# Kernel tuning notes

Measured on AMD Instinct MI355X. Metric: run time of the kernel, lower is better.

## Reference

```python
import jax, jax.numpy as jnp
import numpy as np

B, N, D, G = 128, 36, 512, 2  # batch, num_bboxs, wrd_embed_size, num_glimpses
NEG = -1e10


def setup_inputs() -> dict:
    key = jax.random.key(0)
    k1, k2, k3 = jax.random.split(key, 3)
    obj_repr = jax.random.normal(k1, (B, N, D), dtype=jnp.float32)
    # attn_glimpse[0]: nn.Linear(num_bboxs * wrd_embed_size, num_glimpses)
    W = jax.random.normal(k2, (G, N * D), dtype=jnp.float32) * 0.02
    b = jnp.zeros((G,), dtype=jnp.float32)
    bboxs_mask = jax.random.randint(k3, (B, N), 0, 2).astype(bool)
    bboxs_mask = bboxs_mask.at[:, 0].set(True)  # at least one valid box per row
    return {"obj_repr": obj_repr, "W": W, "b": b, "bboxs_mask": bboxs_mask}


def reference(obj_repr, W, b, bboxs_mask):
    """Faithful port of QGenModel.self_diff_attention."""
    Bv, Nv, Dv = obj_repr.shape
    # pairwise object differences, gated by the query object: [B, N, N, D]
    diff = obj_repr[:, :, None, :] * (obj_repr[:, :, None, :] - obj_repr[:, None, :, :])
    flat = diff.reshape(Bv, Nv, Nv * Dv)              # [B, N, N*D]
    logits = flat @ W.T + b                            # [B, N, G]
    logits = jnp.where(bboxs_mask[:, :, None], logits, NEG)
    weight = jax.nn.softmax(logits, axis=1)            # softmax over box axis (dim=1)
    # weight.transpose(1,2) @ obj_repr  ->  [B, G, D]
    vis_repr = jnp.einsum('bng,bnd->bgd', weight, obj_repr)
    return vis_repr.reshape(Bv, -1)                    # [B, G*D]
```

## Files before the change

kernel.cpp:

```cpp
#include <hip/hip_runtime.h>
#include <hip/hip_bf16.h>


#define QB 128
#define QN 36
#define QD 512
#define QG 2

__global__ __launch_bounds__(QD) void qgen_self_diff_attn(
    const float* __restrict__ obj,
    const float* __restrict__ W,
    const float* __restrict__ bias,
    const int* __restrict__ mask,
    float* __restrict__ out)
{
    __shared__ float s_T[QD];
    __shared__ float s_S[QD];
    __shared__ float s_logit[QN];
    __shared__ float s_w[QN];

    const int bid = blockIdx.x;
    const int b = bid & (QB - 1);
    const int g = bid >> 7;
    const int t = threadIdx.x;
    const int wave = t >> 6;
    const int lane = t & 63;

    const float* ob = obj + (size_t)b * QN * QD;
    const float* wg = W + (size_t)g * QN * QD;

    float o[QN];
    float T = 0.f, S = 0.f;
    #pragma unroll
    for (int m = 0; m < QN; ++m) {
        o[m] = ob[m * QD + t];
        float w = wg[m * QD + t];
        T = fmaf(w, o[m], T);
        S += w;
    }
    s_T[t] = T;
    s_S[t] = S;
    __syncthreads();

    for (int n = wave; n < QN; n += 8) {
        float a = 0.f;
        #pragma unroll
        for (int k = 0; k < QD / 64; ++k) {
            int d = lane + k * 64;
            float ov = ob[n * QD + d];
            a += ov * ov * s_S[d] - ov * s_T[d];
        }
        #pragma unroll
        for (int off = 32; off; off >>= 1)
            a += __shfl_down(a, off);
        if (lane == 0) {
            bool mk = mask[b * QN + n] != 0;
            s_logit[n] = mk ? a + bias[g] : -1e10f;
        }
    }
    __syncthreads();

    if (wave == 0) {
        float v = (lane < QN) ? s_logit[lane] : -1e30f;
        float mx = v;
        #pragma unroll
        for (int off = 32; off; off >>= 1)
            mx = fmaxf(mx, __shfl_xor(mx, off));
        float e = (lane < QN) ? __expf(v - mx) : 0.f;
        float sum = e;
        #pragma unroll
        for (int off = 32; off; off >>= 1)
            sum += __shfl_xor(sum, off);
        if (lane < QN) s_w[lane] = e / sum;
    }
    __syncthreads();

    float v = 0.f;
    #pragma unroll
    for (int n = 0; n < QN; ++n)
        v = fmaf(s_w[n], o[n], v);
    out[(size_t)b * QG * QD + (size_t)g * QD + t] = v;
}

extern "C" void kernel_launch(void* const* d_in, const int* in_sizes, int n_in,
                              void* d_out, int out_size, void* d_ws, size_t ws_size,
                              hipStream_t stream) {
    const float* obj  = (const float*)d_in[0];
    const float* W    = (const float*)d_in[1];
    const float* bias = (const float*)d_in[2];
    const int*   mask = (const int*)d_in[3];
    float* out = (float*)d_out;

    qgen_self_diff_attn<<<QB * QG, QD, 0, stream>>>(obj, W, bias, mask, out);
}
```

Before: 68.05 us.

## Repartition work as float4 row-groups, reuse register tiles for logits

Each block's 512 threads now split into 4 row groups of 128 threads. Each thread holds 9 objects as float4 vectors, loaded with vectorized 16-byte loads. Partial T/S sums are reduced across groups through shared memory. The per-object logits are computed from the register-resident values, so obj is no longer re-read from global memory in the logit loop. The final weighted sum is reduced across groups through shared memory before the store. In exchange the kernel adds an extra shared-memory reduction and sync and more partial-sum shuffles.

```diff
diff --git a/kernel.cpp b/kernel.cpp
--- a/kernel.cpp
+++ b/kernel.cpp
@@ -1,85 +1,124 @@
 #include <hip/hip_runtime.h>
-#include <hip/hip_bf16.h>
 
 
 #define QB 128
 #define QN 36
 #define QD 512
 #define QG 2
+#define NMQ 9
+#define NR 128
 
-__global__ __launch_bounds__(QD) void qgen_self_diff_attn(
+__global__ __launch_bounds__(512) void qgen_self_diff_attn(
     const float* __restrict__ obj,
     const float* __restrict__ W,
     const float* __restrict__ bias,
     const int* __restrict__ mask,
     float* __restrict__ out)
 {
-    __shared__ float s_T[QD];
-    __shared__ float s_S[QD];
-    __shared__ float s_logit[QN];
-    __shared__ float s_w[QN];
+    __shared__ float4 s_T[4][NR];
+    __shared__ float4 s_S[4][NR];
+    __shared__ float  s_lp[8][NMQ];
+    __shared__ float  s_w[QN];
 
-    const int bid = blockIdx.x;
-    const int b = bid & (QB - 1);
-    const int g = bid >> 7;
-    const int t = threadIdx.x;
+    const int bid  = blockIdx.x;
+    const int b    = bid & (QB - 1);
+    const int g    = bid >> 7;
+    const int t    = threadIdx.x;
+    const int q    = t >> 7;
+    const int r    = t & (NR - 1);
     const int wave = t >> 6;
     const int lane = t & 63;
 
-    const float* ob = obj + (size_t)b * QN * QD;
-    const float* wg = W + (size_t)g * QN * QD;
+    int   mk = 1;
+    float bg = 0.f;
+    if (wave == 0) {
+        bg = bias[g];
+        if (lane < QN) mk = mask[b * QN + lane];
+    }
 
-    float o[QN];
-    float T = 0.f, S = 0.f;
+    const float4* ob4 = (const float4*)(obj + (size_t)b * QN * QD);
+    const float4* wg4 = (const float4*)(W   + (size_t)g * QN * QD);
+
+    float4 o[NMQ];
+    float4 Tp = make_float4(0.f, 0.f, 0.f, 0.f);
+    float4 Sp = make_float4(0.f, 0.f, 0.f, 0.f);
     #pragma unroll
-    for (int m = 0; m < QN; ++m) {
-        o[m] = ob[m * QD + t];
-        float w = wg[m * QD + t];
-        T = fmaf(w, o[m], T);
-        S += w;
+    for (int j = 0; j < NMQ; ++j) {
+        const int m = q + 4 * j;
+        const float4 ov = ob4[m * NR + r];
+        const float4 wv = wg4[m * NR + r];
+        o[j] = ov;
+        Tp.x = fmaf(wv.x, ov.x, Tp.x); Tp.y = fmaf(wv.y, ov.y, Tp.y);
+        Tp.z = fmaf(wv.z, ov.z, Tp.z); Tp.w = fmaf(wv.w, ov.w, Tp.w);
+        Sp.x += wv.x; Sp.y += wv.y; Sp.z += wv.z; Sp.w += wv.w;
     }
-    s_T[t] = T;
-    s_S[t] = S;
+    s_T[q][r] = Tp;
+    s_S[q][r] = Sp;
     __syncthreads();
 
-    for (int n = wave; n < QN; n += 8) {
-        float a = 0.f;
-        #pragma unroll
-        for (int k = 0; k < QD / 64; ++k) {
-            int d = lane + k * 64;
-            float ov = ob[n * QD + d];
-            a += ov * ov * s_S[d] - ov * s_T[d];
-        }
+    float4 T = s_T[0][r], S = s_S[0][r];
+    #pragma unroll
+    for (int k = 1; k < 4; ++k) {
+        const float4 a = s_T[k][r], c = s_S[k][r];
+        T.x += a.x; T.y += a.y; T.z += a.z; T.w += a.w;
+        S.x += c.x; S.y += c.y; S.z += c.z; S.w += c.w;
+    }
+
+    float p[NMQ];
+    #pragma unroll
+    for (int j = 0; j < NMQ; ++j) {
+        const float4 ov = o[j];
+        float a;
+        a  = ov.x * fmaf(ov.x, S.x, -T.x);
+        a += ov.y * fmaf(ov.y, S.y, -T.y);
+        a += ov.z * fmaf(ov.z, S.z, -T.z);
+        a += ov.w * fmaf(ov.w, S.w, -T.w);
+        p[j] = a;
+    }
+    #pragma unroll
+    for (int j = 0; j < NMQ; ++j) {
+        float a = p[j];
         #pragma unroll
         for (int off = 32; off; off >>= 1)
             a += __shfl_down(a, off);
-        if (lane == 0) {
-            bool mk = mask[b * QN + n] != 0;
-            s_logit[n] = mk ? a + bias[g] : -1e10f;
-        }
+        if (lane == 0) s_lp[wave][j] = a;
     }
     __syncthreads();
 
     if (wave == 0) {
-        float v = (lane < QN) ? s_logit[lane] : -1e30f;
-        float mx = v;
+        float l = -3e38f;
+        if (lane < QN) {
+            const int nq = lane & 3, nj = lane >> 2;
+            const float v = s_lp[2 * nq][nj] + s_lp[2 * nq + 1][nj];
+            l = mk ? v + bg : -1e10f;
+        }
+        float mx = l;
         #pragma unroll
         for (int off = 32; off; off >>= 1)
             mx = fmaxf(mx, __shfl_xor(mx, off));
-        float e = (lane < QN) ? __expf(v - mx) : 0.f;
-        float sum = e;
+        const float e = (lane < QN) ? __expf(l - mx) : 0.f;
+        float sm = e;
         #pragma unroll
         for (int off = 32; off; off >>= 1)
-            sum += __shfl_xor(sum, off);
-        if (lane < QN) s_w[lane] = e / sum;
+            sm += __shfl_xor(sm, off);
+        if (lane < QN) s_w[lane] = e / sm;
     }
     __syncthreads();
 
-    float v = 0.f;
+    float4 acc = make_float4(0.f, 0.f, 0.f, 0.f);
     #pragma unroll
-    for (int n = 0; n < QN; ++n)
-        v = fmaf(s_w[n], o[n], v);
-    out[(size_t)b * QG * QD + (size_t)g * QD + t] = v;
+    for (int j = 0; j < NMQ; ++j) {
+        const float wn = s_w[q + 4 * j];
+        const float4 ov = o[j];
+        acc.x = fmaf(wn, ov.x, acc.x); acc.y = fmaf(wn, ov.y, acc.y);
+        acc.z = fmaf(wn, ov.z, acc.z); acc.w = fmaf(wn, ov.w, acc.w);
+    }
+    s_T[q][r] = acc;
+    __syncthreads();
+
+    const float* sv = (const float*)&s_T[0][0];
+    const float v = sv[t] + sv[512 + t] + sv[1024 + t] + sv[1536 + t];
+    out[(size_t)b * (QG * QD) + (size_t)g * QD + t] = v;
 }
 
 extern "C" void kernel_launch(void* const* d_in, const int* in_sizes, int n_in,
@@ -91,5 +130,5 @@
     const int*   mask = (const int*)d_in[3];
     float* out = (float*)d_out;
 
-    qgen_self_diff_attn<<<QB * QG, QD, 0, stream>>>(obj, W, bias, mask, out);
+    qgen_self_diff_attn<<<QB * QG, 512, 0, stream>>>(obj, W, bias, mask, out);
 }
```

Result: faster. 66.51 us (-2.3%).
